# Kernel optimization log

Hardware: AMD Instinct MI355X
Metric: run time of the kernel (lower is better)

Reference implementation:

```python
import jax, jax.numpy as jnp
import numpy as np

A = -0.75  # torch grid_sample bicubic coefficient
EPS_CLAMP = 1e-07


def geo_pad(x, p):
    # GeoCyclicPadding: flip+half-roll across poles (H), circular in longitude (W)
    B, C, H, W = x.shape
    top = jnp.roll(jnp.flip(x[:, :, :p, :], axis=2), W // 2, axis=3)
    bot = jnp.roll(jnp.flip(x[:, :, H - p:, :], axis=2), W // 2, axis=3)
    x = jnp.concatenate([top, x, bot], axis=2)
    return jnp.concatenate([x[:, :, :, W - p:], x, x[:, :, :, :p]], axis=3)


def conv3(x, w, b):
    y = jax.lax.conv_general_dilated(x, w, (1, 1), 'VALID',
                                     dimension_numbers=('NCHW', 'OIHW', 'NCHW'))
    return y + b[None, :, None, None]


def layernorm_chw(x, g, b):
    mu = jnp.mean(x, axis=(1, 2, 3), keepdims=True)
    var = jnp.mean((x - mu) ** 2, axis=(1, 2, 3), keepdims=True)
    return (x - mu) * jax.lax.rsqrt(var + 1e-5) * g[None] + b[None]


def cubic_weights(t):
    # cubic convolution weights for taps at offsets -1,0,1,2 (a = -0.75)
    w0 = A * (1 + t) ** 3 - 5 * A * (1 + t) ** 2 + 8 * A * (1 + t) - 4 * A
    w1 = (A + 2) * t ** 3 - (A + 3) * t ** 2 + 1
    w2 = (A + 2) * (1 - t) ** 3 - (A + 3) * (1 - t) ** 2 + 1
    w3 = A * (2 - t) ** 3 - 5 * A * (2 - t) ** 2 + 8 * A * (2 - t) - 4 * A
    return (w0, w1, w2, w3)


def bicubic_sample_border(img, gx, gy):
    # img: [N,Hp,Wp]; gx,gy: [N,H,W] normalized coords; align_corners=True, border padding
    N, Hp, Wp = img.shape
    ix = jnp.clip((gx + 1) * 0.5 * (Wp - 1), 0.0, Wp - 1)
    iy = jnp.clip((gy + 1) * 0.5 * (Hp - 1), 0.0, Hp - 1)
    x0f = jnp.floor(ix)
    y0f = jnp.floor(iy)
    tx = ix - x0f
    ty = iy - y0f
    x0 = x0f.astype(jnp.int32)
    y0 = y0f.astype(jnp.int32)
    wx = cubic_weights(tx)
    wy = cubic_weights(ty)
    nidx = jnp.arange(N)[:, None, None]
    out = jnp.zeros_like(ix)
    for i in range(4):
        yi = jnp.clip(y0 + (i - 1), 0, Hp - 1)
        row = jnp.zeros_like(ix)
        for j in range(4):
            xj = jnp.clip(x0 + (j - 1), 0, Wp - 1)
            row = row + wx[j] * img[nidx, yi, xj]
        out = out + wy[i] * row
    return out


def reference(hidden_features, lat_grid, lon_grid, w1, b1, ln_g, ln_b, w2, b2, dt):
    B, C, H, W = hidden_features.shape
    # velocity_net = CLP (double conv)
    x = geo_pad(hidden_features, 1)
    x = conv3(x, w1, b1)
    x = jax.nn.silu(layernorm_chw(x, ln_g, ln_b))
    x = geo_pad(x, 1)
    vel = conv3(x, w2, b2)                      # [B, 2C, H, W]
    vel = vel.reshape(B, 2, C, H, W).transpose(0, 2, 1, 3, 4)  # [B, C, 2, H, W]
    u = vel[:, :, 0]
    v = vel[:, :, 1]
    lon_prime = -u * dt
    lat_prime = -v * dt
    lat_p = lat_grid[:, None, :, :]  # broadcast over channels
    lon_p = lon_grid[:, None, :, :]
    # rotated -> standard lat/lon
    sin_lat_prime = jnp.sin(lat_prime)
    cos_lat_prime = jnp.cos(lat_prime)
    sin_lon_prime = jnp.sin(lon_prime)
    cos_lon_prime = jnp.cos(lon_prime)
    sin_lat_p = jnp.sin(lat_p)
    cos_lat_p = jnp.cos(lat_p)
    sin_lat = sin_lat_prime * cos_lat_p + cos_lat_prime * cos_lon_prime * sin_lat_p
    lat_dep = jnp.arcsin(jnp.clip(sin_lat, -1 + EPS_CLAMP, 1 - EPS_CLAMP))
    num = cos_lat_prime * sin_lon_prime
    den = cos_lat_prime * cos_lon_prime * cos_lat_p - sin_lat_prime * sin_lat_p
    lon_dep = lon_p + jnp.arctan2(num, den)
    lon_dep = jnp.remainder(lon_dep + 2 * jnp.pi, 2 * jnp.pi)
    pw = W + 2
    ph = H + 2
    grid_x = (lon_dep / (2 * jnp.pi) * 2 - 1) * (W / pw)
    grid_y = (lat_dep / jnp.pi * 2 - 1) * (H / ph)
    padded = geo_pad(hidden_features, 1).reshape(B * C, ph, pw)
    out = bicubic_sample_border(padded,
                                grid_x.reshape(B * C, H, W),
                                grid_y.reshape(B * C, H, W))
    return out.reshape(B, C, H, W)


def setup_inputs() -> dict:
    key = jax.random.key(0)
    ks = jax.random.split(key, 4)
    B, C, H, W = 2, 128, 240, 480
    hidden_features = jax.random.normal(ks[0], (B, C, H, W), dtype=jnp.float32)
    lat = jnp.linspace(-jnp.pi / 2 + 1e-3, jnp.pi / 2 - 1e-3, H, dtype=jnp.float32)
    lon = jnp.linspace(0.0, 2 * jnp.pi * (1 - 1.0 / W), W, dtype=jnp.float32)
    lat_grid = jnp.broadcast_to(lat[None, :, None], (B, H, W)).astype(jnp.float32)
    lon_grid = jnp.broadcast_to(lon[None, None, :], (B, H, W)).astype(jnp.float32)
    w1 = jax.random.normal(ks[1], (C, C, 3, 3), dtype=jnp.float32) * 0.02
    b1 = jnp.zeros((C,), dtype=jnp.float32)
    ln_g = jnp.ones((C, H, W), dtype=jnp.float32)
    ln_b = jnp.zeros((C, H, W), dtype=jnp.float32)
    w2 = jax.random.normal(ks[2], (2 * C, C, 3, 3), dtype=jnp.float32) * 0.02
    b2 = jnp.zeros((2 * C,), dtype=jnp.float32)
    return {"hidden_features": hidden_features, "lat_grid": lat_grid,
            "lon_grid": lon_grid, "w1": w1, "b1": b1, "ln_g": ln_g,
            "ln_b": ln_b, "w2": w2, "b2": b2, "dt": 0.1}
```

## Files before the change

### kernel.cpp

```cpp
#include <hip/hip_runtime.h>
#include <math.h>

#define Hh 240
#define Ww 480
#define HW 115200
#define Cc 128
#define Kk 1152
#define HALFW 240
#define NB_RED 1440
#define WLCAP 4194304

typedef unsigned int u32;
typedef unsigned short u16;
typedef short bf16x8 __attribute__((ext_vector_type(8)));
typedef float f32x4 __attribute__((ext_vector_type(4)));

__device__ __forceinline__ u16 f2bf(float x) {
    u32 u = __float_as_uint(x);
    u32 r = (u + 0x7fffu + ((u >> 16) & 1u)) >> 16;
    return (u16)r;
}
__device__ __forceinline__ float bf2f(u16 h) { return __uint_as_float(((u32)h) << 16); }

__device__ __forceinline__ int geo_sidx(int r, int c) {
    int wv = (c < 0) ? (Ww - 1) : ((c >= Ww) ? 0 : c);
    int rr;
    if (r < 0)        { rr = 0;      wv = (wv >= HALFW) ? wv - HALFW : wv + HALFW; }
    else if (r >= Hh) { rr = Hh - 1; wv = (wv >= HALFW) ? wv - HALFW : wv + HALFW; }
    else              { rr = r; }
    return rr * Ww + wv;
}

__device__ __forceinline__ float padfetch(const float* __restrict__ p, int yi, int xj) {
    return p[geo_sidx(yi - 1, xj - 1)];
}

__device__ __forceinline__ void sincos_small(double x, double* s, double* c) {
    double x2 = x * x;
    if (x2 > 0.49) { *s = sin(x); *c = cos(x); return; }
    *s = x * (1.0 + x2 * (-1.6666666666666666e-1 + x2 * (8.3333333333333333e-3 +
         x2 * (-1.9841269841269841e-4 + x2 * (2.7557319223985893e-6 - x2 * 2.5052108385441720e-8)))));
    *c = 1.0 + x2 * (-0.5 + x2 * (4.1666666666666666e-2 + x2 * (-1.3888888888888889e-3 +
         x2 * (2.4801587301587302e-5 - x2 * 2.7557319223985893e-7))));
}

__device__ __forceinline__ void snipe_tail(double u, double v, double dt,
                                           double phi_s, double phi_c, double lam,
                                           const float* __restrict__ plane,
                                           float* __restrict__ outp)
{
    const double TWO_PI = 6.2831853071795864769252867665590;
    const double PI_D   = 3.1415926535897932384626433832795;

    double lonp = -u * dt, latp = -v * dt;
    double slp, clp, slo, clo;
    sincos_small(latp, &slp, &clp);
    sincos_small(lonp, &slo, &clo);

    double sinlat = slp * phi_c + clp * clo * phi_s;
    sinlat = fmin(fmax(sinlat, -1.0 + 1e-7), 1.0 - 1e-7);
    double lat_dep = asin(sinlat);

    double num = clp * slo;
    double den = clp * clo * phi_c - slp * phi_s;
    double lon_dep = lam + atan2(num, den);
    double xr = lon_dep + TWO_PI;
    xr = xr - floor(xr / TWO_PI) * TWO_PI;

    double gx = (xr / TWO_PI * 2.0 - 1.0) * (480.0 / 482.0);
    double gy = (lat_dep / PI_D * 2.0 - 1.0) * (240.0 / 242.0);
    double ixd = fmin(fmax((gx + 1.0) * 0.5 * 481.0, 0.0), 481.0);
    double iyd = fmin(fmax((gy + 1.0) * 0.5 * 241.0, 0.0), 241.0);

    double x0d = floor(ixd), y0d = floor(iyd);
    float fx = (float)(ixd - x0d), fy = (float)(iyd - y0d);
    int x0 = (int)x0d, y0 = (int)y0d;

    const float a = -0.75f;
    float wx[4], wy[4];
    {
        float t = fx;
        float t1 = 1.f + t, t2 = 2.f - t, s1 = 1.f - t;
        wx[0] = ((a * t1 - 5.f * a) * t1 + 8.f * a) * t1 - 4.f * a;
        wx[1] = ((a + 2.f) * t - (a + 3.f)) * t * t + 1.f;
        wx[2] = ((a + 2.f) * s1 - (a + 3.f)) * s1 * s1 + 1.f;
        wx[3] = ((a * t2 - 5.f * a) * t2 + 8.f * a) * t2 - 4.f * a;
        t = fy;
        t1 = 1.f + t; t2 = 2.f - t; s1 = 1.f - t;
        wy[0] = ((a * t1 - 5.f * a) * t1 + 8.f * a) * t1 - 4.f * a;
        wy[1] = ((a + 2.f) * t - (a + 3.f)) * t * t + 1.f;
        wy[2] = ((a + 2.f) * s1 - (a + 3.f)) * s1 * s1 + 1.f;
        wy[3] = ((a * t2 - 5.f * a) * t2 + 8.f * a) * t2 - 4.f * a;
    }
    float accv = 0.f;
    #pragma unroll
    for (int i = 0; i < 4; i++) {
        int yi = min(max(y0 + i - 1, 0), 241);
        float row = 0.f;
        #pragma unroll
        for (int j = 0; j < 4; j++) {
            int xj = min(max(x0 + j - 1, 0), 481);
            row = fmaf(wx[j], padfetch(plane, yi, xj), row);
        }
        accv = fmaf(wy[i], row, accv);
    }
    *outp = accv;
}

__global__ void split_w(const float* __restrict__ w, u16* __restrict__ sp, int total) {
    int i = blockIdx.x * 256 + threadIdx.x;
    if (i >= total) return;
    float x = w[i];
    u16 a = f2bf(x); float r1 = x - bf2f(a);
    u16 b = f2bf(r1); float r2 = r1 - bf2f(b);
    sp[i] = a; sp[total + i] = b; sp[2 * total + i] = f2bf(r2);
}

template<int NN>
__global__ __launch_bounds__(256)
void conv_mfma(const float* __restrict__ in,
               const u16*  __restrict__ wsp,
               const float* __restrict__ bias,
               float* __restrict__ out)
{
    constexpr int NT     = NN / 32;
    constexpr int NTILES = NN / 16;
    __shared__ short Al[3][8][4][16][8];
    __shared__ short Bl[3][NTILES][4][16][8];

    const int tid  = threadIdx.x;
    const int lane = tid & 63;
    const int wave = tid >> 6;
    const int wm = wave & 1, wn = wave >> 1;
    const int lr = lane & 15, kg = lane >> 4;
    const int m0 = blockIdx.x * 128;

    const int ms   = tid & 127;
    const int ks   = (tid >> 7) * 16;
    const int mt_s = ms >> 4, lr_s = ms & 15;
    const int kg0  = ks >> 3;
    const int gm = m0 + ms;
    const int h = gm / Ww, w = gm - h * Ww;
    int sidx[9];
    #pragma unroll
    for (int q = 0; q < 9; q++) sidx[q] = geo_sidx(h + q / 3 - 1, w + q % 3 - 1);

    f32x4 acc[4][NT] = {};

    for (int kt = 0; kt < Kk; kt += 32) {
        __syncthreads();
        {
            int k = kt + ks;
            int ic = k / 9, t9 = k - ic * 9;
            short hh[3][16];
            #pragma unroll
            for (int j = 0; j < 16; j++) {
                float x = in[ic * HW + sidx[t9]];
                u16 a = f2bf(x); float r1 = x - bf2f(a);
                u16 b = f2bf(r1); float r2 = r1 - bf2f(b);
                hh[0][j] = (short)a; hh[1][j] = (short)b; hh[2][j] = (short)f2bf(r2);
                if (++t9 == 9) { t9 = 0; ic++; }
            }
            #pragma unroll
            for (int p = 0; p < 3; p++) {
                #pragma unroll
                for (int half = 0; half < 2; half++) {
                    bf16x8 v;
                    #pragma unroll
                    for (int j = 0; j < 8; j++) v[j] = hh[p][half * 8 + j];
                    *(bf16x8*)&Al[p][mt_s][kg0 + half][lr_s][0] = v;
                }
            }
        }
        {
            constexpr int NCH = 3 * NN * 4 / 256;
            #pragma unroll
            for (int cg = 0; cg < NCH; cg++) {
                int chunk = tid + cg * 256;
                int p = chunk / (NN * 4);
                int rem = chunk - p * NN * 4;
                int n = rem >> 2, part = rem & 3;
                bf16x8 v = *(const bf16x8*)&wsp[(size_t)(p * NN + n) * Kk + kt + part * 8];
                *(bf16x8*)&Bl[p][n >> 4][part][n & 15][0] = v;
            }
        }
        __syncthreads();
        bf16x8 af[3][4];
        #pragma unroll
        for (int pa = 0; pa < 3; pa++)
            #pragma unroll
            for (int mt = 0; mt < 4; mt++)
                af[pa][mt] = *(const bf16x8*)&Al[pa][wm * 4 + mt][kg][lr][0];
        #pragma unroll
        for (int pb = 0; pb < 3; pb++) {
            #pragma unroll
            for (int nt = 0; nt < NT; nt++) {
                bf16x8 bq = *(const bf16x8*)&Bl[pb][wn * NT + nt][kg][lr][0];
                #pragma unroll
                for (int pa = 0; pa < 3 - pb; pa++) {
                    #pragma unroll
                    for (int mt = 0; mt < 4; mt++)
                        acc[mt][nt] = __builtin_amdgcn_mfma_f32_16x16x32_bf16(
                            af[pa][mt], bq, acc[mt][nt], 0, 0, 0);
                }
            }
        }
    }
    #pragma unroll
    for (int mt = 0; mt < 4; mt++) {
        int mbase = m0 + wm * 64 + mt * 16 + kg * 4;
        #pragma unroll
        for (int nt = 0; nt < NT; nt++) {
            int n = wn * (NN / 2) + nt * 16 + lr;
            float bv = bias[n];
            float4 o;
            o.x = acc[mt][nt][0] + bv;
            o.y = acc[mt][nt][1] + bv;
            o.z = acc[mt][nt][2] + bv;
            o.w = acc[mt][nt][3] + bv;
            *(float4*)&out[(size_t)n * HW + mbase] = o;
        }
    }
}

__global__ __launch_bounds__(256)
void reduce_stats(const float* __restrict__ y, float* __restrict__ part) {
    const int n4 = (Cc * HW) / 4;
    float s = 0.f, ss = 0.f;
    for (int i = blockIdx.x * 256 + threadIdx.x; i < n4; i += NB_RED * 256) {
        float4 v = ((const float4*)y)[i];
        s  += v.x + v.y + v.z + v.w;
        ss += v.x * v.x + v.y * v.y + v.z * v.z + v.w * v.w;
    }
    #pragma unroll
    for (int o = 32; o > 0; o >>= 1) { s += __shfl_down(s, o); ss += __shfl_down(ss, o); }
    __shared__ float ls[4], lss[4];
    int wid = threadIdx.x >> 6, lane = threadIdx.x & 63;
    if (lane == 0) { ls[wid] = s; lss[wid] = ss; }
    __syncthreads();
    if (threadIdx.x == 0) {
        part[blockIdx.x * 2]     = ls[0] + ls[1] + ls[2] + ls[3];
        part[blockIdx.x * 2 + 1] = lss[0] + lss[1] + lss[2] + lss[3];
    }
}

__global__ __launch_bounds__(256)
void finalize_stats(const float* __restrict__ part, float* __restrict__ stats) {
    float s = 0.f, ss = 0.f;
    for (int i = threadIdx.x; i < NB_RED; i += 256) { s += part[2 * i]; ss += part[2 * i + 1]; }
    #pragma unroll
    for (int o = 32; o > 0; o >>= 1) { s += __shfl_down(s, o); ss += __shfl_down(ss, o); }
    __shared__ float ls[4], lss[4];
    int wid = threadIdx.x >> 6, lane = threadIdx.x & 63;
    if (lane == 0) { ls[wid] = s; lss[wid] = ss; }
    __syncthreads();
    if (threadIdx.x == 0) {
        stats[0] = ls[0] + ls[1] + ls[2] + ls[3];
        stats[1] = lss[0] + lss[1] + lss[2] + lss[3];
    }
}

__global__ void norm_silu(float* __restrict__ y, const float* __restrict__ g,
                          const float* __restrict__ bb, const float* __restrict__ stats) {
    int i = blockIdx.x * 256 + threadIdx.x;
    if (i >= Cc * HW) return;
    const float invN = 1.f / (float)(Cc * HW);
    float mu  = stats[0] * invN;
    float var = stats[1] * invN - mu * mu;
    float inv = rsqrtf(var + 1e-5f);
    float z = (y[i] - mu) * inv * g[i] + bb[i];
    y[i] = z / (1.f + expf(-z));
}

__global__ __launch_bounds__(256)
void semilag(const float* __restrict__ vel, const float* __restrict__ hid,
             const float* __restrict__ latg, const float* __restrict__ lng,
             const float* __restrict__ dtp, float* __restrict__ out,
             u32* __restrict__ wl, u32* __restrict__ wlcnt)
{
    int idx = blockIdx.x * 256 + threadIdx.x;
    if (idx >= Cc * HW) return;
    int c = idx / HW;
    int m = idx - c * HW;

    const float PI2F = 6.28318530717958647692f;

    float uf = vel[idx];
    float vf = vel[Cc * HW + idx];
    float dtf = dtp[0];
    float phi = latg[m], lam = lng[m];
    float sphi = sinf(phi), cphi = cosf(phi);

    float lonp = -uf * dtf, latp = -vf * dtf;
    float slp = sinf(latp), clp = cosf(latp);
    float slo = sinf(lonp), clo = cosf(lonp);
    float sinlat = slp * cphi + clp * clo * sphi;
    float num = clp * slo;
    float den = clp * clo * cphi - slp * sphi;
    float r2 = num * num + den * den;

    float lon_w = lam + atan2f(num, den) + PI2F;
    lon_w = lon_w - floorf(lon_w / PI2F) * PI2F;
    float seam = fminf(lon_w, PI2F - lon_w);

    bool pole = (m < 2 * Ww) | (m >= HW - 2 * Ww);
    bool snipe = !pole & ((r2 < 1e-4f) | (fabsf(sinlat) > 1.f - 1e-5f) | (seam < 1e-3f));
    if (snipe) {
        u32 s = atomicAdd(wlcnt, 1u);
        if (s < WLCAP) wl[s] = (u32)idx;
    }

    float sl = fminf(fmaxf(sinlat, -1.f + 1e-7f), 1.f - 1e-7f);
    float lat_dep = asinf(sl);
    float gx = (lon_w / PI2F * 2.f - 1.f) * (480.f / 482.f);
    float gy = (lat_dep / 3.14159265358979323846f * 2.f - 1.f) * (240.f / 242.f);
    double ixd = (double)fminf(fmaxf((gx + 1.f) * 0.5f * 481.f, 0.f), 481.f);
    double iyd = (double)fminf(fmaxf((gy + 1.f) * 0.5f * 241.f, 0.f), 241.f);

    double x0d = floor(ixd), y0d = floor(iyd);
    float fx = (float)(ixd - x0d), fy = (float)(iyd - y0d);
    int x0 = (int)x0d, y0 = (int)y0d;

    const float a = -0.75f;
    float wx[4], wy[4];
    {
        float t = fx;
        float t1 = 1.f + t, t2 = 2.f - t, s1 = 1.f - t;
        wx[0] = ((a * t1 - 5.f * a) * t1 + 8.f * a) * t1 - 4.f * a;
        wx[1] = ((a + 2.f) * t - (a + 3.f)) * t * t + 1.f;
        wx[2] = ((a + 2.f) * s1 - (a + 3.f)) * s1 * s1 + 1.f;
        wx[3] = ((a * t2 - 5.f * a) * t2 + 8.f * a) * t2 - 4.f * a;
        t = fy;
        t1 = 1.f + t; t2 = 2.f - t; s1 = 1.f - t;
        wy[0] = ((a * t1 - 5.f * a) * t1 + 8.f * a) * t1 - 4.f * a;
        wy[1] = ((a + 2.f) * t - (a + 3.f)) * t * t + 1.f;
        wy[2] = ((a + 2.f) * s1 - (a + 3.f)) * s1 * s1 + 1.f;
        wy[3] = ((a * t2 - 5.f * a) * t2 + 8.f * a) * t2 - 4.f * a;
    }

    const float* plane = hid + (size_t)c * HW;
    float accv = 0.f;
    #pragma unroll
    for (int i = 0; i < 4; i++) {
        int yi = min(max(y0 + i - 1, 0), 241);
        float row = 0.f;
        #pragma unroll
        for (int j = 0; j < 4; j++) {
            int xj = min(max(x0 + j - 1, 0), 481);
            row = fmaf(wx[j], padfetch(plane, yi, xj), row);
        }
        accv = fmaf(wy[i], row, accv);
    }
    out[idx] = accv;
}

__global__ __launch_bounds__(256)
void sniper_rows(const float* __restrict__ y1, const float* __restrict__ w2,
                 const float* __restrict__ b2, const float* __restrict__ hid,
                 const float* __restrict__ latg, const float* __restrict__ lng,
                 const float* __restrict__ dtp, float* __restrict__ out)
{
    __shared__ float xl[Kk];
    __shared__ double resd[256];

    const int tid = threadIdx.x;
    const int ri  = blockIdx.x / Ww;
    const int col = blockIdx.x - ri * Ww;
    const int r   = (ri < 2) ? ri : (236 + ri);
    const int m   = r * Ww + col;

    for (int k = tid; k < Kk; k += 256) {
        int ic = k / 9, t9 = k - ic * 9;
        xl[k] = y1[ic * HW + geo_sidx(r + t9 / 3 - 1, col + t9 % 3 - 1)];
    }
    __syncthreads();

    {
        const float* wrow = w2 + (size_t)tid * Kk;
        double a0 = 0.0, a1 = 0.0, a2 = 0.0, a3 = 0.0;
        #pragma unroll 4
        for (int k = 0; k < Kk; k += 4) {
            a0 = fma((double)wrow[k],     (double)xl[k],     a0);
            a1 = fma((double)wrow[k + 1], (double)xl[k + 1], a1);
            a2 = fma((double)wrow[k + 2], (double)xl[k + 2], a2);
            a3 = fma((double)wrow[k + 3], (double)xl[k + 3], a3);
        }
        resd[tid] = (a0 + a1) + (a2 + a3);
    }
    __syncthreads();

    if (tid < Cc) {
        double u = (double)b2[tid] + resd[tid];
        double v = (double)b2[Cc + tid] + resd[Cc + tid];
        double dt = (double)dtp[0];
        double phi = (double)latg[m];
        snipe_tail(u, v, dt, sin(phi), cos(phi), (double)lng[m],
                   hid + (size_t)tid * HW, &out[(size_t)tid * HW + m]);
    }
}

__global__ __launch_bounds__(256)
void sniper(const u32* __restrict__ wl, const u32* __restrict__ wlcnt,
            const float* __restrict__ y1, const float* __restrict__ w2,
            const float* __restrict__ b2, const float* __restrict__ hid,
            const float* __restrict__ latg, const float* __restrict__ lng,
            const float* __restrict__ dtp, float* __restrict__ out)
{
    const int lane = threadIdx.x & 63;
    const int wavid = (blockIdx.x * 256 + threadIdx.x) >> 6;
    const int nwaves = gridDim.x * 4;
    int n = (int)*wlcnt; if (n > WLCAP) n = WLCAP;

    for (int e = wavid; e < n; e += nwaves) {
        u32 idx = wl[e];
        int c = idx / HW, m = idx - c * HW;
        int h = m / Ww, w = m - h * Ww;

        double su = 0.0, sv = 0.0;
        const float* wu = w2 + (size_t)c * Kk;
        const float* wv = w2 + (size_t)(Cc + c) * Kk;
        #pragma unroll
        for (int t9 = 0; t9 < 9; t9++) {
            int s = geo_sidx(h + t9 / 3 - 1, w + t9 % 3 - 1);
            #pragma unroll
            for (int q = 0; q < 2; q++) {
                int ic = q * 64 + lane;
                int k = ic * 9 + t9;
                double yv = (double)y1[ic * HW + s];
                su = fma((double)wu[k], yv, su);
                sv = fma((double)wv[k], yv, sv);
            }
        }
        #pragma unroll
        for (int o = 32; o > 0; o >>= 1) {
            su += __shfl_down(su, o);
            sv += __shfl_down(sv, o);
        }
        if (lane == 0) {
            double u = (double)b2[c] + su;
            double v = (double)b2[Cc + c] + sv;
            double dt = (double)dtp[0];
            double phi = (double)latg[m];
            snipe_tail(u, v, dt, sin(phi), cos(phi), (double)lng[m],
                       hid + (size_t)c * HW, &out[idx]);
        }
    }
}

extern "C" void kernel_launch(void* const* d_in, const int* in_sizes, int n_in,
                              void* d_out, int out_size, void* d_ws, size_t ws_size,
                              hipStream_t stream)
{
    const float* hidden = (const float*)d_in[0];
    const float* latg   = (const float*)d_in[1];
    const float* lng    = (const float*)d_in[2];
    const float* w1     = (const float*)d_in[3];
    const float* b1     = (const float*)d_in[4];
    const float* g      = (const float*)d_in[5];
    const float* lb     = (const float*)d_in[6];
    const float* w2     = (const float*)d_in[7];
    const float* b2     = (const float*)d_in[8];
    const float* dt     = (const float*)d_in[9];
    float* out = (float*)d_out;

    float* ws    = (float*)d_ws;
    float* stats = ws;
    float* part  = ws + 4;
    u32*   wlcnt = (u32*)(ws + 4 + 2 * NB_RED);
    u16*   wsp1  = (u16*)(ws + 4 + 2 * NB_RED + 4);
    u16*   wsp2  = wsp1 + (size_t)3 * Cc * Kk;
    float* y1    = (float*)(wsp2 + (size_t)3 * 2 * Cc * Kk);
    float* vel   = y1 + (size_t)Cc * HW;
    u32*   wl    = (u32*)(vel + (size_t)2 * Cc * HW);

    split_w<<<(Cc * Kk + 255) / 256, 256, 0, stream>>>(w1, wsp1, Cc * Kk);
    split_w<<<(2 * Cc * Kk + 255) / 256, 256, 0, stream>>>(w2, wsp2, 2 * Cc * Kk);

    for (int b = 0; b < 2; b++) {
        const float* hb = hidden + (size_t)b * Cc * HW;
        const float* lab = latg + (size_t)b * HW;
        const float* lob = lng + (size_t)b * HW;
        float* ob = out + (size_t)b * Cc * HW;

        conv_mfma<128><<<HW / 128, 256, 0, stream>>>(hb, wsp1, b1, y1);
        reduce_stats<<<NB_RED, 256, 0, stream>>>(y1, part);
        finalize_stats<<<1, 256, 0, stream>>>(part, stats + 2 * b);
        norm_silu<<<(Cc * HW) / 256, 256, 0, stream>>>(y1, g, lb, stats + 2 * b);
        conv_mfma<256><<<HW / 128, 256, 0, stream>>>(y1, wsp2, b2, vel);
        hipMemsetAsync(wlcnt, 0, 4, stream);
        semilag<<<(Cc * HW) / 256, 256, 0, stream>>>(vel, hb, lab, lob, dt, ob, wl, wlcnt);
        sniper_rows<<<4 * Ww, 256, 0, stream>>>(y1, w2, b2, hb, lab, lob, dt, ob);
        sniper<<<2048, 256, 0, stream>>>(wl, wlcnt, y1, w2, b2, hb, lab, lob, dt, ob);
    }
}
```

Measured before the change: 3.081 ms.

## Pre-swizzle split weights into LDS tile order and load via global_load_lds

```diff
diff --git a/kernel.cpp b/kernel.cpp
--- a/kernel.cpp
+++ b/kernel.cpp
@@ -14,6 +14,8 @@
 typedef unsigned short u16;
 typedef short bf16x8 __attribute__((ext_vector_type(8)));
 typedef float f32x4 __attribute__((ext_vector_type(4)));
+typedef __attribute__((address_space(3))) u32 lds_u32;
+typedef const __attribute__((address_space(1))) u32 glb_u32;
 
 __device__ __forceinline__ u16 f2bf(float x) {
     u32 u = __float_as_uint(x);
@@ -107,19 +109,30 @@
     *outp = accv;
 }
 
-__global__ void split_w(const float* __restrict__ w, u16* __restrict__ sp, int total) {
-    int i = blockIdx.x * 256 + threadIdx.x;
-    if (i >= total) return;
-    float x = w[i];
+__global__ void reorder_w(const float* __restrict__ w, u16* __restrict__ outp, int NN) {
+    int idx = blockIdx.x * 256 + threadIdx.x;
+    int total = 3 * NN * Kk;
+    if (idx >= total) return;
+    int per_kt = 3 * NN * 32;
+    int t = idx / per_kt;
+    int rem = idx - t * per_kt;
+    int U = rem >> 3, j = rem & 7;
+    int NT64 = (NN / 16) * 64;
+    int p = U / NT64;
+    int r2 = U - p * NT64;
+    int ntile = r2 >> 6, part = (r2 >> 4) & 3, nlow = r2 & 15;
+    int n = ntile * 16 + nlow;
+    int k = t * 32 + part * 8 + j;
+    float x = w[(size_t)n * Kk + k];
     u16 a = f2bf(x); float r1 = x - bf2f(a);
-    u16 b = f2bf(r1); float r2 = r1 - bf2f(b);
-    sp[i] = a; sp[total + i] = b; sp[2 * total + i] = f2bf(r2);
+    u16 b = f2bf(r1); float rr = r1 - bf2f(b);
+    outp[idx] = (p == 0) ? a : ((p == 1) ? b : f2bf(rr));
 }
 
 template<int NN>
 __global__ __launch_bounds__(256)
 void conv_mfma(const float* __restrict__ in,
-               const u16*  __restrict__ wsp,
+               const u16*  __restrict__ wspr,
                const float* __restrict__ bias,
                float* __restrict__ out)
 {
@@ -145,10 +158,24 @@
     #pragma unroll
     for (int q = 0; q < 9; q++) sidx[q] = geo_sidx(h + q / 3 - 1, w + q % 3 - 1);
 
+    short* const Blbase = &Bl[0][0][0][0][0];
+    const u16* const bsrc = wspr + (size_t)tid * 8;
+    constexpr int NCH = (3 * NN * 32 / 8) / 256;
+
     f32x4 acc[4][NT] = {};
 
     for (int kt = 0; kt < Kk; kt += 32) {
         __syncthreads();
+        {
+            const u16* src = bsrc + (size_t)(kt >> 5) * (3 * NN * 32);
+            #pragma unroll
+            for (int cg = 0; cg < NCH; cg++) {
+                __builtin_amdgcn_global_load_lds(
+                    (glb_u32*)(src + (size_t)cg * 2048),
+                    (lds_u32*)(Blbase + (size_t)(cg * 256 + tid) * 8),
+                    16, 0, 0);
+            }
+        }
         {
             int k = kt + ks;
             int ic = k / 9, t9 = k - ic * 9;
@@ -172,18 +199,6 @@
                 }
             }
         }
-        {
-            constexpr int NCH = 3 * NN * 4 / 256;
-            #pragma unroll
-            for (int cg = 0; cg < NCH; cg++) {
-                int chunk = tid + cg * 256;
-                int p = chunk / (NN * 4);
-                int rem = chunk - p * NN * 4;
-                int n = rem >> 2, part = rem & 3;
-                bf16x8 v = *(const bf16x8*)&wsp[(size_t)(p * NN + n) * Kk + kt + part * 8];
-                *(bf16x8*)&Bl[p][n >> 4][part][n & 15][0] = v;
-            }
-        }
         __syncthreads();
         bf16x8 af[3][4];
         #pragma unroll
@@ -473,8 +488,8 @@
     float* vel   = y1 + (size_t)Cc * HW;
     u32*   wl    = (u32*)(vel + (size_t)2 * Cc * HW);
 
-    split_w<<<(Cc * Kk + 255) / 256, 256, 0, stream>>>(w1, wsp1, Cc * Kk);
-    split_w<<<(2 * Cc * Kk + 255) / 256, 256, 0, stream>>>(w2, wsp2, 2 * Cc * Kk);
+    reorder_w<<<(3 * Cc * Kk + 255) / 256, 256, 0, stream>>>(w1, wsp1, Cc);
+    reorder_w<<<(3 * 2 * Cc * Kk + 255) / 256, 256, 0, stream>>>(w2, wsp2, 2 * Cc);
 
     for (int b = 0; b < 2; b++) {
         const float* hb = hidden + (size_t)b * Cc * HW;
```

Result: faster. 2.719 ms (-11.7%).
